# Optimization experiments

Measured on AMD Instinct MI355X. Metric: run time of the kernel, lower is better.

Reference implementation:

```python
import jax, jax.numpy as jnp
import numpy as np

B, T, S = 4, 2048, 2048
D, H, DFF = 1024, 16, 4096
HD = D // H
EPS = 1e-5


def layer_norm(x, gamma, beta):
    mean = x.mean(-1, keepdims=True)
    var = ((x - mean) ** 2).mean(-1, keepdims=True)
    return gamma * (x - mean) / jnp.sqrt(var + EPS) + beta


def attn(q, k, v):
    # q: [B,H,Tq,hd], k,v: [B,H,Tk,hd]
    scores = jnp.einsum('bhqd,bhkd->bhqk', q, k) / (HD ** 0.5)
    p = jax.nn.softmax(scores, axis=-1)
    return jnp.einsum('bhqk,bhkd->bhqd', p, v)


def split_heads(x, n_chunks):
    # x: [B,T,n_chunks*D] -> n_chunks tensors [B,H,T,hd] (matches torch reshape/chunk order)
    b, t, _ = x.shape
    x = x.reshape(b, t, H, n_chunks * HD).transpose(0, 2, 1, 3)
    return jnp.split(x, n_chunks, axis=-1)


def merge_heads(x):
    b, h, t, hd = x.shape
    return x.transpose(0, 2, 1, 3).reshape(b, t, h * hd)


def setup_inputs() -> dict:
    key = jax.random.key(0)
    ks = jax.random.split(key, 16)
    s = 0.02
    return {
        'x_enc': jax.random.normal(ks[0], (B, S, D), jnp.float32),
        'x_dec': jax.random.normal(ks[1], (B, T, D), jnp.float32),
        'qkv_w': jax.random.normal(ks[2], (D, 3 * D), jnp.float32) * s,
        'qkv_b': jnp.zeros((3 * D,), jnp.float32),
        'sa_o_w': jax.random.normal(ks[3], (D, D), jnp.float32) * s,
        'sa_o_b': jnp.zeros((D,), jnp.float32),
        'g1': jnp.ones((D,), jnp.float32),
        'be1': jnp.zeros((D,), jnp.float32),
        'q_w': jax.random.normal(ks[4], (D, D), jnp.float32) * s,
        'q_b': jnp.zeros((D,), jnp.float32),
        'kv_w': jax.random.normal(ks[5], (D, 2 * D), jnp.float32) * s,
        'kv_b': jnp.zeros((2 * D,), jnp.float32),
        'ca_o_w': jax.random.normal(ks[6], (D, D), jnp.float32) * s,
        'ca_o_b': jnp.zeros((D,), jnp.float32),
        'g2': jnp.ones((D,), jnp.float32),
        'be2': jnp.zeros((D,), jnp.float32),
        'ff_w1': jax.random.normal(ks[7], (D, DFF), jnp.float32) * s,
        'ff_b1': jnp.zeros((DFF,), jnp.float32),
        'ff_w2': jax.random.normal(ks[8], (DFF, D), jnp.float32) * s,
        'ff_b2': jnp.zeros((D,), jnp.float32),
        'g3': jnp.ones((D,), jnp.float32),
        'be3': jnp.zeros((D,), jnp.float32),
    }


def reference(x_enc, x_dec, qkv_w, qkv_b, sa_o_w, sa_o_b, g1, be1,
              q_w, q_b, kv_w, kv_b, ca_o_w, ca_o_b, g2, be2,
              ff_w1, ff_b1, ff_w2, ff_b2, g3, be3):
    # --- self attention on x_dec (dropout = identity at inference) ---
    qkv = x_dec @ qkv_w + qkv_b                      # [B,T,3D]
    q, k, v = split_heads(qkv, 3)
    sa = merge_heads(attn(q, k, v)) @ sa_o_w + sa_o_b
    res = layer_norm(sa + x_dec, g1, be1)
    # --- cross attention: q from decoder stream, kv from encoder ---
    kv = x_enc @ kv_w + kv_b                         # [B,S,2D]
    kc, vc = split_heads(kv, 2)
    qc, = split_heads(res @ q_w + q_b, 1)
    ca = merge_heads(attn(qc, kc, vc)) @ ca_o_w + ca_o_b
    res2 = layer_norm(ca + res, g2, be2)
    # --- feed forward ---
    ff = jax.nn.relu(res2 @ ff_w1 + ff_b1) @ ff_w2 + ff_b2
    return layer_norm(ff + res2, g3, be3)
```

## Files before the change

kernel.cpp:

```cpp
#include <hip/hip_runtime.h>

typedef unsigned short u16;
typedef unsigned int   u32;
typedef __bf16 bf16_t;
typedef bf16_t bf16x4 __attribute__((ext_vector_type(4)));
typedef bf16_t bf16x8 __attribute__((ext_vector_type(8)));
typedef float  f32x4  __attribute__((ext_vector_type(4)));

__device__ __forceinline__ u16 f2bf(float f) {
  u32 u = __builtin_bit_cast(u32, f);
  u32 r = u + 0x7fffu + ((u >> 16) & 1u);
  return (u16)(r >> 16);
}
__device__ __forceinline__ float bf2f(u16 h) {
  u32 u = ((u32)h) << 16;
  return __builtin_bit_cast(float, u);
}

__device__ __forceinline__ void gl_lds16(const u16* g, u16* l) {
  __builtin_amdgcn_global_load_lds(
      (const __attribute__((address_space(1))) u32*)g,
      (__attribute__((address_space(3))) u32*)l, 16, 0, 0);
}

__global__ __launch_bounds__(256) void k_cvt(const float* __restrict__ in,
                                             u16* __restrict__ out, long n4) {
  long i = (long)blockIdx.x * 256 + threadIdx.x;
  if (i >= n4) return;
  float4 v = reinterpret_cast<const float4*>(in)[i];
  ushort4 o;
  o.x = f2bf(v.x); o.y = f2bf(v.y); o.z = f2bf(v.z); o.w = f2bf(v.w);
  reinterpret_cast<ushort4*>(out)[i] = o;
}

__global__ __launch_bounds__(256) void k_transpose_cvt(const float* __restrict__ W,
                                                       u16* __restrict__ Wt,
                                                       int K, int N) {
  __shared__ u16 tile[32][33];
  int n0 = blockIdx.x * 32, k0 = blockIdx.y * 32;
  int tx = threadIdx.x & 31, ty = threadIdx.x >> 5;
#pragma unroll
  for (int i = 0; i < 4; ++i) {
    int k = ty + i * 8;
    tile[k][tx] = f2bf(W[(size_t)(k0 + k) * N + n0 + tx]);
  }
  __syncthreads();
#pragma unroll
  for (int i = 0; i < 4; ++i) {
    int n = ty + i * 8;
    Wt[(size_t)(n0 + n) * K + k0 + tx] = tile[tx][n];
  }
}

__global__ __launch_bounds__(256) void k_vtrans(const u16* __restrict__ in,
                                                u16* __restrict__ out,
                                                long long ibs, int ihs, int irs,
                                                int Tk) {
  __shared__ u16 t[64][72];
  const int tid = threadIdx.x;
  const int head = blockIdx.y;
  const int b = head >> 4, h = head & 15;
  const int kt = blockIdx.x * 64;
  const u16* ip = in + (size_t)b * ibs + (size_t)h * ihs;
  u16* op = out + (size_t)head * 64 * Tk;
#pragma unroll
  for (int i = 0; i < 2; ++i) {
    int c = i * 256 + tid;
    int key = c >> 3, d = (c & 7) * 8;
    *reinterpret_cast<uint4*>(&t[key][d]) =
        *reinterpret_cast<const uint4*>(ip + (size_t)(kt + key) * irs + d);
  }
  __syncthreads();
#pragma unroll
  for (int i = 0; i < 2; ++i) {
    int c = i * 256 + tid;
    int d = c >> 3, k8 = (c & 7) * 8;
    ushort4 lo, hi;
    lo.x = t[k8 + 0][d]; lo.y = t[k8 + 1][d]; lo.z = t[k8 + 2][d]; lo.w = t[k8 + 3][d];
    hi.x = t[k8 + 4][d]; hi.y = t[k8 + 5][d]; hi.z = t[k8 + 6][d]; hi.w = t[k8 + 7][d];
    uint4 o;
    o.x = ((u32)lo.y << 16) | lo.x; o.y = ((u32)lo.w << 16) | lo.z;
    o.z = ((u32)hi.y << 16) | hi.x; o.w = ((u32)hi.w << 16) | hi.z;
    *reinterpret_cast<uint4*>(op + (size_t)d * Tk + kt + k8) = o;
  }
}

template<int RELU>
__global__ __launch_bounds__(256) void k_gemm_bt(
    const u16* __restrict__ A, const u16* __restrict__ Bt,
    const float* __restrict__ bias, u16* __restrict__ C,
    int M, int N, int K)
{
  __shared__ __align__(16) u16 As[2][128 * 64];
  __shared__ __align__(16) u16 Bs[2][128 * 64];
  const int tid = threadIdx.x;
  const int lane = tid & 63, wid = tid >> 6;
  const int wr = wid >> 1, wc = wid & 1;
  const int l15 = lane & 15, g = lane >> 4;
  const int bm = blockIdx.x * 128, bn = blockIdx.y * 128;
  const int srow = lane >> 3, scol = (lane & 7) * 8;

  f32x4 acc[4][4] = {};

  auto stage = [&](int buf, int kt) {
#pragma unroll
    for (int i = 0; i < 4; ++i) {
      int ch = wid * 4 + i;
      gl_lds16(A  + (size_t)(bm + ch * 8 + srow) * K + kt + scol, &As[buf][ch * 512]);
      gl_lds16(Bt + (size_t)(bn + ch * 8 + srow) * K + kt + scol, &Bs[buf][ch * 512]);
    }
  };

  stage(0, 0);
  __syncthreads();
  int cur = 0;
  for (int kt = 0; kt < K; kt += 64) {
    if (kt + 64 < K) stage(cur ^ 1, kt + 64);
#pragma unroll
    for (int ks = 0; ks < 2; ++ks) {
      bf16x8 af[4], bfr[4];
#pragma unroll
      for (int m = 0; m < 4; ++m)
        af[m] = *reinterpret_cast<const bf16x8*>(&As[cur][(wr * 64 + m * 16 + l15) * 64 + ks * 32 + g * 8]);
#pragma unroll
      for (int n = 0; n < 4; ++n)
        bfr[n] = *reinterpret_cast<const bf16x8*>(&Bs[cur][(wc * 64 + n * 16 + l15) * 64 + ks * 32 + g * 8]);
      __builtin_amdgcn_s_setprio(1);
#pragma unroll
      for (int m = 0; m < 4; ++m)
#pragma unroll
        for (int n = 0; n < 4; ++n)
          acc[m][n] = __builtin_amdgcn_mfma_f32_16x16x32_bf16(af[m], bfr[n], acc[m][n], 0, 0, 0);
      __builtin_amdgcn_s_setprio(0);
    }
    __syncthreads();
    cur ^= 1;
  }
  float bv[4];
#pragma unroll
  for (int n = 0; n < 4; ++n) bv[n] = bias[bn + wc * 64 + n * 16 + l15];
#pragma unroll
  for (int m = 0; m < 4; ++m)
#pragma unroll
    for (int r = 0; r < 4; ++r) {
      int row = bm + wr * 64 + m * 16 + g * 4 + r;
#pragma unroll
      for (int n = 0; n < 4; ++n) {
        float v = acc[m][n][r] + bv[n];
        if (RELU) v = fmaxf(v, 0.f);
        C[(size_t)row * N + bn + wc * 64 + n * 16 + l15] = f2bf(v);
      }
    }
}

__global__ __launch_bounds__(256) void k_gemm_sk(
    const u16* __restrict__ A, const u16* __restrict__ Bt,
    float* __restrict__ P,
    int M, int N, int Kfull, int Kchunk)
{
  __shared__ __align__(16) u16 As[2][128 * 32];
  __shared__ __align__(16) u16 Bs[2][128 * 32];
  const int tid = threadIdx.x;
  const int lane = tid & 63, wid = tid >> 6;
  const int wr = wid >> 1, wc = wid & 1;
  const int l15 = lane & 15, g = lane >> 4;
  const int bm = blockIdx.x * 128, bn = blockIdx.y * 128;
  const int z = blockIdx.z;
  const int k0 = z * Kchunk;
  float* Pz = P + (size_t)z * M * N;
  const int srow = tid >> 2, scol = (tid & 3) * 8;

  f32x4 acc[4][4] = {};

  auto stage = [&](int buf, int kt) {
#pragma unroll
    for (int i = 0; i < 2; ++i) {
      int row = i * 64 + srow;
      gl_lds16(A  + (size_t)(bm + row) * Kfull + k0 + kt + scol, &As[buf][row * 32 + scol]);
      gl_lds16(Bt + (size_t)(bn + row) * Kfull + k0 + kt + scol, &Bs[buf][row * 32 + scol]);
    }
  };

  stage(0, 0);
  __syncthreads();
  int cur = 0;
  for (int kt = 0; kt < Kchunk; kt += 32) {
    if (kt + 32 < Kchunk) stage(cur ^ 1, kt + 32);
    bf16x8 af[4], bfr[4];
#pragma unroll
    for (int m = 0; m < 4; ++m)
      af[m] = *reinterpret_cast<const bf16x8*>(&As[cur][(wr * 64 + m * 16 + l15) * 32 + g * 8]);
#pragma unroll
    for (int n = 0; n < 4; ++n)
      bfr[n] = *reinterpret_cast<const bf16x8*>(&Bs[cur][(wc * 64 + n * 16 + l15) * 32 + g * 8]);
    __builtin_amdgcn_s_setprio(1);
#pragma unroll
    for (int m = 0; m < 4; ++m)
#pragma unroll
      for (int n = 0; n < 4; ++n)
        acc[m][n] = __builtin_amdgcn_mfma_f32_16x16x32_bf16(af[m], bfr[n], acc[m][n], 0, 0, 0);
    __builtin_amdgcn_s_setprio(0);
    __syncthreads();
    cur ^= 1;
  }
#pragma unroll
  for (int m = 0; m < 4; ++m)
#pragma unroll
    for (int r = 0; r < 4; ++r) {
      int row = bm + wr * 64 + m * 16 + g * 4 + r;
#pragma unroll
      for (int n = 0; n < 4; ++n)
        Pz[(size_t)row * N + bn + wc * 64 + n * 16 + l15] = acc[m][n][r];
    }
}

template<int RELU>
__global__ __launch_bounds__(512, 1) void k_gemm256(
    const u16* __restrict__ A, const u16* __restrict__ Bt,
    const float* __restrict__ bias, u16* __restrict__ C,
    int M, int N, int K)
{
  __shared__ __align__(16) u16 lds[65536];
  const int tid = threadIdx.x;
  const int lane = tid & 63, wid = tid >> 6;
  const int wr = wid >> 2, wc = wid & 3;
  const int l15 = lane & 15, g = lane >> 4;
  const int bm = blockIdx.x * 256, bn = blockIdx.y * 256;
  const int srow = tid >> 3;
  const int swcol = (((tid & 7) ^ ((tid >> 3) & 7)) * 8);
  const int swr = l15 & 7;

  f32x4 acc[8][4] = {};

  auto stageA = [&](int buf, int j, int kt) {
    gl_lds16(A + (size_t)(bm + j * 64 + srow) * K + kt + swcol,
             lds + buf * 32768 + j * 4096 + wid * 512);
  };
  auto stageB = [&](int buf, int j, int kt) {
    gl_lds16(Bt + (size_t)(bn + j * 64 + srow) * K + kt + swcol,
             lds + buf * 32768 + 16384 + j * 4096 + wid * 512);
  };

  stageB(0, 0, 0); stageB(0, 1, 0); stageB(0, 2, 0); stageB(0, 3, 0);
  stageA(0, 0, 0); stageA(0, 2, 0); stageA(0, 1, 0); stageA(0, 3, 0);
  asm volatile("s_waitcnt vmcnt(2)" ::: "memory");
  __builtin_amdgcn_s_barrier();

  int cur = 0;
  for (int kt = 0; kt < K; kt += 64) {
    const u16* Ab = lds + cur * 32768;
    const u16* Bb = lds + cur * 32768 + 16384;
    const bool pre = (kt + 64 < K);
    const int nb = cur ^ 1;
    bf16x8 af[4][2], bflo[2][2], bfhi[2][2];

#pragma unroll
    for (int m = 0; m < 4; ++m)
#pragma unroll
      for (int ks = 0; ks < 2; ++ks)
        af[m][ks] = *reinterpret_cast<const bf16x8*>(
            &Ab[(2 * wr) * 4096 + (m * 16 + l15) * 64 + (((ks * 4 + g) ^ swr) * 8)]);
#pragma unroll
    for (int n = 0; n < 2; ++n)
#pragma unroll
      for (int ks = 0; ks < 2; ++ks)
        bflo[n][ks] = *reinterpret_cast<const bf16x8*>(
            &Bb[wc * 4096 + (n * 16 + l15) * 64 + (((ks * 4 + g) ^ swr) * 8)]);
    if (pre) { stageB(nb, 0, kt + 64); stageB(nb, 1, kt + 64); }
    __builtin_amdgcn_s_setprio(1);
#pragma unroll
    for (int m = 0; m < 4; ++m)
#pragma unroll
      for (int n = 0; n < 2; ++n)
#pragma unroll
        for (int ks = 0; ks < 2; ++ks)
          acc[m][n] = __builtin_amdgcn_mfma_f32_16x16x32_bf16(af[m][ks], bflo[n][ks], acc[m][n], 0, 0, 0);
    __builtin_amdgcn_s_setprio(0);
    __builtin_amdgcn_s_barrier();

#pragma unroll
    for (int n = 0; n < 2; ++n)
#pragma unroll
      for (int ks = 0; ks < 2; ++ks)
        bfhi[n][ks] = *reinterpret_cast<const bf16x8*>(
            &Bb[wc * 4096 + ((n + 2) * 16 + l15) * 64 + (((ks * 4 + g) ^ swr) * 8)]);
    if (pre) { stageB(nb, 2, kt + 64); stageB(nb, 3, kt + 64); }
    __builtin_amdgcn_s_setprio(1);
#pragma unroll
    for (int m = 0; m < 4; ++m)
#pragma unroll
      for (int n = 0; n < 2; ++n)
#pragma unroll
        for (int ks = 0; ks < 2; ++ks)
          acc[m][n + 2] = __builtin_amdgcn_mfma_f32_16x16x32_bf16(af[m][ks], bfhi[n][ks], acc[m][n + 2], 0, 0, 0);
    __builtin_amdgcn_s_setprio(0);
    if (pre) { asm volatile("s_waitcnt vmcnt(4)" ::: "memory"); }
    else     { asm volatile("s_waitcnt vmcnt(0)" ::: "memory"); }
    __builtin_amdgcn_s_barrier();

#pragma unroll
    for (int m = 0; m < 4; ++m)
#pragma unroll
      for (int ks = 0; ks < 2; ++ks)
        af[m][ks] = *reinterpret_cast<const bf16x8*>(
            &Ab[(2 * wr + 1) * 4096 + (m * 16 + l15) * 64 + (((ks * 4 + g) ^ swr) * 8)]);
    if (pre) { stageA(nb, 0, kt + 64); stageA(nb, 2, kt + 64); }
    __builtin_amdgcn_s_setprio(1);
#pragma unroll
    for (int m = 0; m < 4; ++m)
#pragma unroll
      for (int n = 0; n < 2; ++n)
#pragma unroll
        for (int ks = 0; ks < 2; ++ks)
          acc[m + 4][n + 2] = __builtin_amdgcn_mfma_f32_16x16x32_bf16(af[m][ks], bfhi[n][ks], acc[m + 4][n + 2], 0, 0, 0);
    __builtin_amdgcn_s_setprio(0);
    __builtin_amdgcn_s_barrier();

    if (pre) { stageA(nb, 1, kt + 64); stageA(nb, 3, kt + 64); }
    __builtin_amdgcn_s_setprio(1);
#pragma unroll
    for (int m = 0; m < 4; ++m)
#pragma unroll
      for (int n = 0; n < 2; ++n)
#pragma unroll
        for (int ks = 0; ks < 2; ++ks)
          acc[m + 4][n] = __builtin_amdgcn_mfma_f32_16x16x32_bf16(af[m][ks], bflo[n][ks], acc[m + 4][n], 0, 0, 0);
    __builtin_amdgcn_s_setprio(0);
    asm volatile("s_waitcnt vmcnt(2)" ::: "memory");
    __builtin_amdgcn_s_barrier();
    cur ^= 1;
  }

  float bv[4];
#pragma unroll
  for (int n = 0; n < 4; ++n) bv[n] = bias[bn + wc * 64 + n * 16 + l15];
#pragma unroll
  for (int m = 0; m < 8; ++m)
#pragma unroll
    for (int r = 0; r < 4; ++r) {
      int row = bm + wr * 128 + m * 16 + g * 4 + r;
#pragma unroll
      for (int n = 0; n < 4; ++n) {
        float v = acc[m][n][r] + bv[n];
        if (RELU) v = fmaxf(v, 0.f);
        C[(size_t)row * N + bn + wc * 64 + n * 16 + l15] = f2bf(v);
      }
    }
}

__global__ __launch_bounds__(512) void k_flash2(
    const u16* __restrict__ Qg, const u16* __restrict__ Kg, const u16* __restrict__ VTg,
    u16* __restrict__ Og,
    long long qbs, int qhs, int qrs,
    long long kbs, int khs, int krs,
    long long obs, int ohs, int ors,
    int Tk)
{
  __shared__ __align__(16) u16 Ks[64][72];
  __shared__ __align__(16) u16 Vs[64][72];
  const int tid = threadIdx.x;
  const int lane = tid & 63, wid = tid >> 6;
  const int l15 = lane & 15, g = lane >> 4;
  const int head = blockIdx.x;
  const int b = head >> 4, h = head & 15;
  const int srow = tid >> 3, scol = (tid & 7) * 8;

  const u16* Q  = Qg + (size_t)b * qbs + (size_t)h * qhs;
  const u16* Kp = Kg + (size_t)b * kbs + (size_t)h * khs;
  const u16* Vp = VTg + (size_t)head * 64 * Tk;
  u16* Op = Og + (size_t)b * obs + (size_t)h * ohs;

  const int q0 = blockIdx.y * 256 + wid * 32;
  const float SCL = 0.125f * 1.44269504f;

  bf16x8 qf0[2], qf1[2];
#pragma unroll
  for (int ks = 0; ks < 2; ++ks) {
    bf16x8 r0 = *reinterpret_cast<const bf16x8*>(Q + (size_t)(q0 + l15) * qrs + ks * 32 + g * 8);
    bf16x8 r1 = *reinterpret_cast<const bf16x8*>(Q + (size_t)(q0 + 16 + l15) * qrs + ks * 32 + g * 8);
#pragma unroll
    for (int j = 0; j < 8; ++j) {
      qf0[ks][j] = (bf16_t)((float)r0[j] * SCL);
      qf1[ks][j] = (bf16_t)((float)r1[j] * SCL);
    }
  }
  bf16x8 ones;
#pragma unroll
  for (int j = 0; j < 8; ++j) ones[j] = (bf16_t)1.0f;

  f32x4 oacc0[4] = {}, oacc1[4] = {};
  f32x4 lacc0 = {}, lacc1 = {};

  uint4 ka, va, kb, vb;

  auto load_set = [&](int kt, uint4& k0, uint4& v0) {
    k0 = *reinterpret_cast<const uint4*>(Kp + (size_t)(kt + srow) * krs + scol);
    v0 = *reinterpret_cast<const uint4*>(Vp + (size_t)srow * Tk + kt + scol);
  };

  auto tile = [&](const uint4& k0, const uint4& v0,
                  int ktn, uint4& nk0, uint4& nv0) {
    __syncthreads();
    *reinterpret_cast<uint4*>(&Ks[srow][scol]) = k0;
    *reinterpret_cast<uint4*>(&Vs[srow][scol]) = v0;
    load_set(ktn, nk0, nv0);
    __syncthreads();

    f32x4 sc0[4] = {}, sc1[4] = {};
    __builtin_amdgcn_s_setprio(1);
#pragma unroll
    for (int ks = 0; ks < 2; ++ks)
#pragma unroll
      for (int kb2 = 0; kb2 < 4; ++kb2) {
        bf16x8 kf = *reinterpret_cast<const bf16x8*>(&Ks[kb2 * 16 + l15][ks * 32 + g * 8]);
        sc0[kb2] = __builtin_amdgcn_mfma_f32_16x16x32_bf16(kf, qf0[ks], sc0[kb2], 0, 0, 0);
        sc1[kb2] = __builtin_amdgcn_mfma_f32_16x16x32_bf16(kf, qf1[ks], sc1[kb2], 0, 0, 0);
      }
    __builtin_amdgcn_s_setprio(0);

    bf16x8 p0a, p0b, p1a, p1b;
#pragma unroll
    for (int r = 0; r < 4; ++r) {
      p0a[r]     = (bf16_t)__builtin_amdgcn_exp2f(sc0[0][r]);
      p0a[4 + r] = (bf16_t)__builtin_amdgcn_exp2f(sc0[1][r]);
      p0b[r]     = (bf16_t)__builtin_amdgcn_exp2f(sc0[2][r]);
      p0b[4 + r] = (bf16_t)__builtin_amdgcn_exp2f(sc0[3][r]);
      p1a[r]     = (bf16_t)__builtin_amdgcn_exp2f(sc1[0][r]);
      p1a[4 + r] = (bf16_t)__builtin_amdgcn_exp2f(sc1[1][r]);
      p1b[r]     = (bf16_t)__builtin_amdgcn_exp2f(sc1[2][r]);
      p1b[4 + r] = (bf16_t)__builtin_amdgcn_exp2f(sc1[3][r]);
    }

    __builtin_amdgcn_s_setprio(1);
#pragma unroll
    for (int kc = 0; kc < 2; ++kc) {
      const bf16x8& pf0 = kc ? p0b : p0a;
      const bf16x8& pf1 = kc ? p1b : p1a;
#pragma unroll
      for (int nb = 0; nb < 4; ++nb) {
        bf16x4 vlo = *reinterpret_cast<const bf16x4*>(&Vs[nb * 16 + l15][kc * 32 + 4 * g]);
        bf16x4 vhi = *reinterpret_cast<const bf16x4*>(&Vs[nb * 16 + l15][kc * 32 + 16 + 4 * g]);
        bf16x8 vf;
#pragma unroll
        for (int j = 0; j < 4; ++j) { vf[j] = vlo[j]; vf[4 + j] = vhi[j]; }
        oacc0[nb] = __builtin_amdgcn_mfma_f32_16x16x32_bf16(pf0, vf, oacc0[nb], 0, 0, 0);
        oacc1[nb] = __builtin_amdgcn_mfma_f32_16x16x32_bf16(pf1, vf, oacc1[nb], 0, 0, 0);
      }
      lacc0 = __builtin_amdgcn_mfma_f32_16x16x32_bf16(pf0, ones, lacc0, 0, 0, 0);
      lacc1 = __builtin_amdgcn_mfma_f32_16x16x32_bf16(pf1, ones, lacc1, 0, 0, 0);
    }
    __builtin_amdgcn_s_setprio(0);
  };

  load_set(0, ka, va);
  for (int kt = 0; kt < Tk; kt += 128) {
    tile(ka, va, kt + 64, kb, vb);
    int ktn = (kt + 128 < Tk) ? kt + 128 : 0;
    tile(kb, vb, ktn, ka, va);
  }

#pragma unroll
  for (int r = 0; r < 4; ++r) {
    float inv0 = 1.f / lacc0[r];
    float inv1 = 1.f / lacc1[r];
#pragma unroll
    for (int nb = 0; nb < 4; ++nb) {
      Op[(size_t)(q0 + g * 4 + r) * ors + nb * 16 + l15]      = f2bf(oacc0[nb][r] * inv0);
      Op[(size_t)(q0 + 16 + g * 4 + r) * ors + nb * 16 + l15] = f2bf(oacc1[nb][r] * inv1);
    }
  }
}

__device__ __forceinline__ void load4v(const float* p, float* v) {
  float4 t = *reinterpret_cast<const float4*>(p);
  v[0] = t.x; v[1] = t.y; v[2] = t.z; v[3] = t.w;
}
__device__ __forceinline__ void load4v(const u16* p, float* v) {
  ushort4 t = *reinterpret_cast<const ushort4*>(p);
  v[0] = bf2f(t.x); v[1] = bf2f(t.y); v[2] = bf2f(t.z); v[3] = bf2f(t.w);
}
__device__ __forceinline__ void store4v(float* p, const float* v) {
  float4 t; t.x = v[0]; t.y = v[1]; t.z = v[2]; t.w = v[3];
  *reinterpret_cast<float4*>(p) = t;
}
__device__ __forceinline__ void store4v(u16* p, const float* v) {
  ushort4 t; t.x = f2bf(v[0]); t.y = f2bf(v[1]); t.z = f2bf(v[2]); t.w = f2bf(v[3]);
  *reinterpret_cast<ushort4*>(p) = t;
}

__device__ __forceinline__ void ln_core(float* v, int tid, const float* gamma,
                                        const float* beta, float* o) {
  float s = v[0] + v[1] + v[2] + v[3];
  float q = v[0]*v[0] + v[1]*v[1] + v[2]*v[2] + v[3]*v[3];
#pragma unroll
  for (int off = 32; off > 0; off >>= 1) {
    s += __shfl_down(s, off);
    q += __shfl_down(q, off);
  }
  __shared__ float sh[8];
  const int lane = tid & 63, wid = tid >> 6;
  if (lane == 0) { sh[wid] = s; sh[4 + wid] = q; }
  __syncthreads();
  s = sh[0] + sh[1] + sh[2] + sh[3];
  q = sh[4] + sh[5] + sh[6] + sh[7];
  float mean = s * (1.f / 1024.f);
  float var = q * (1.f / 1024.f) - mean * mean;
  float inv = 1.f / sqrtf(var + 1e-5f);
  float gv[4], bv[4];
  load4v(gamma + tid * 4, gv);
  load4v(beta + tid * 4, bv);
#pragma unroll
  for (int j = 0; j < 4; ++j) o[j] = gv[j] * (v[j] - mean) * inv + bv[j];
}

template<typename TRES, typename TOUT>
__global__ __launch_bounds__(256) void k_add_ln(
    const u16* __restrict__ X, const TRES* __restrict__ R,
    const float* __restrict__ gamma, const float* __restrict__ beta,
    TOUT* __restrict__ Out)
{
  const int row = blockIdx.x;
  const int tid = threadIdx.x;
  const size_t base = (size_t)row * 1024 + tid * 4;
  float x[4], rr[4], v[4], o[4];
  load4v(X + base, x);
  load4v(R + base, rr);
#pragma unroll
  for (int j = 0; j < 4; ++j) v[j] = x[j] + rr[j];
  ln_core(v, tid, gamma, beta, o);
  store4v(Out + base, o);
}

__global__ __launch_bounds__(256) void k_add_ln_ff(
    const float* __restrict__ P0, const float* __restrict__ P1,
    const float* __restrict__ bias, const u16* __restrict__ R,
    const float* __restrict__ gamma, const float* __restrict__ beta,
    float* __restrict__ Out)
{
  const int row = blockIdx.x;
  const int tid = threadIdx.x;
  const size_t base = (size_t)row * 1024 + tid * 4;
  float p0[4], p1[4], bb[4], rr[4], v[4], o[4];
  load4v(P0 + base, p0);
  load4v(P1 + base, p1);
  load4v(bias + tid * 4, bb);
  load4v(R + base, rr);
#pragma unroll
  for (int j = 0; j < 4; ++j) v[j] = p0[j] + p1[j] + bb[j] + rr[j];
  ln_core(v, tid, gamma, beta, o);
  store4v(Out + base, o);
}

extern "C" void kernel_launch(void* const* d_in, const int* in_sizes, int n_in,
                              void* d_out, int out_size, void* d_ws, size_t ws_size,
                              hipStream_t stream)
{
  (void)in_sizes; (void)n_in; (void)out_size; (void)ws_size;
  const float* x_enc  = (const float*)d_in[0];
  const float* x_dec  = (const float*)d_in[1];
  const float* qkv_w  = (const float*)d_in[2];
  const float* qkv_b  = (const float*)d_in[3];
  const float* sa_o_w = (const float*)d_in[4];
  const float* sa_o_b = (const float*)d_in[5];
  const float* g1     = (const float*)d_in[6];
  const float* be1    = (const float*)d_in[7];
  const float* q_w    = (const float*)d_in[8];
  const float* q_b    = (const float*)d_in[9];
  const float* kv_w   = (const float*)d_in[10];
  const float* kv_b   = (const float*)d_in[11];
  const float* ca_o_w = (const float*)d_in[12];
  const float* ca_o_b = (const float*)d_in[13];
  const float* g2     = (const float*)d_in[14];
  const float* be2    = (const float*)d_in[15];
  const float* ff_w1  = (const float*)d_in[16];
  const float* ff_b1  = (const float*)d_in[17];
  const float* ff_w2  = (const float*)d_in[18];
  const float* ff_b2  = (const float*)d_in[19];
  const float* g3     = (const float*)d_in[20];
  const float* be3    = (const float*)d_in[21];
  float* out = (float*)d_out;

  u16* Wb = (u16*)d_ws;
  const size_t O_WQKV = 0;
  const size_t O_WSAO = O_WQKV + (size_t)3072 * 1024;
  const size_t O_WQ   = O_WSAO + (size_t)1024 * 1024;
  const size_t O_WKV  = O_WQ   + (size_t)1024 * 1024;
  const size_t O_WCAO = O_WKV  + (size_t)2048 * 1024;
  const size_t O_WFF1 = O_WCAO + (size_t)1024 * 1024;
  const size_t O_WFF2 = O_WFF1 + (size_t)4096 * 1024;
  const size_t O_XD   = O_WFF2 + (size_t)1024 * 4096;
  const size_t O_XE   = O_XD + 8388608;
  const size_t O_QKV  = O_XE + 8388608;
  const size_t O_QC   = O_QKV + 16777216;
  const size_t O_ATT  = O_QKV + 25165824;
  const size_t O_RES  = O_ATT + 8388608;
  const size_t O_RES2 = O_RES + 8388608;
  const size_t O_FF1  = O_RES2 + 8388608;
  const size_t O_VT   = O_FF1;
  const size_t O_VT2  = O_FF1 + 8388608;
  const size_t O_GO   = O_FF1 + 33554432;
  float* Pf = (float*)(Wb + O_QKV);

  k_cvt<<<8192, 256, 0, stream>>>(x_dec, Wb + O_XD, 2097152);
  k_cvt<<<8192, 256, 0, stream>>>(x_enc, Wb + O_XE, 2097152);
  k_transpose_cvt<<<dim3(96, 32),  256, 0, stream>>>(qkv_w,  Wb + O_WQKV, 1024, 3072);
  k_transpose_cvt<<<dim3(32, 32),  256, 0, stream>>>(sa_o_w, Wb + O_WSAO, 1024, 1024);
  k_transpose_cvt<<<dim3(32, 32),  256, 0, stream>>>(q_w,    Wb + O_WQ,   1024, 1024);
  k_transpose_cvt<<<dim3(64, 32),  256, 0, stream>>>(kv_w,   Wb + O_WKV,  1024, 2048);
  k_transpose_cvt<<<dim3(32, 32),  256, 0, stream>>>(ca_o_w, Wb + O_WCAO, 1024, 1024);
  k_transpose_cvt<<<dim3(128, 32), 256, 0, stream>>>(ff_w1,  Wb + O_WFF1, 1024, 4096);
  k_transpose_cvt<<<dim3(32, 128), 256, 0, stream>>>(ff_w2,  Wb + O_WFF2, 4096, 1024);

  k_gemm256<0><<<dim3(32, 12), 512, 0, stream>>>(Wb + O_XD, Wb + O_WQKV, qkv_b,
                                                 Wb + O_QKV, 8192, 3072, 1024);
  k_vtrans<<<dim3(32, 64), 256, 0, stream>>>(Wb + O_QKV + 128, Wb + O_VT,
                                             (long long)2048 * 3072, 192, 3072, 2048);
  k_flash2<<<dim3(64, 8), 512, 0, stream>>>(Wb + O_QKV, Wb + O_QKV + 64, Wb + O_VT,
                                            Wb + O_ATT,
                                            (long long)2048 * 3072, 192, 3072,
                                            (long long)2048 * 3072, 192, 3072,
                                            (long long)2048 * 1024, 64, 1024, 2048);
  k_gemm_bt<0><<<dim3(64, 8), 256, 0, stream>>>(Wb + O_ATT, Wb + O_WSAO, sa_o_b,
                                                Wb + O_GO, 8192, 1024, 1024);
  k_add_ln<float, u16><<<8192, 256, 0, stream>>>(Wb + O_GO, x_dec, g1, be1, Wb + O_RES);

  k_gemm256<0><<<dim3(32, 8), 512, 0, stream>>>(Wb + O_XE, Wb + O_WKV, kv_b,
                                                Wb + O_QKV, 8192, 2048, 1024);
  k_vtrans<<<dim3(32, 64), 256, 0, stream>>>(Wb + O_QKV + 64, Wb + O_VT2,
                                             (long long)2048 * 2048, 128, 2048, 2048);
  k_gemm_bt<0><<<dim3(64, 8), 256, 0, stream>>>(Wb + O_RES, Wb + O_WQ, q_b,
                                                Wb + O_QC, 8192, 1024, 1024);
  k_flash2<<<dim3(64, 8), 512, 0, stream>>>(Wb + O_QC, Wb + O_QKV, Wb + O_VT2,
                                            Wb + O_ATT,
                                            (long long)2048 * 1024, 64, 1024,
                                            (long long)2048 * 2048, 128, 2048,
                                            (long long)2048 * 1024, 64, 1024, 2048);
  k_gemm_bt<0><<<dim3(64, 8), 256, 0, stream>>>(Wb + O_ATT, Wb + O_WCAO, ca_o_b,
                                                Wb + O_GO, 8192, 1024, 1024);
  k_add_ln<u16, u16><<<8192, 256, 0, stream>>>(Wb + O_GO, Wb + O_RES, g2, be2, Wb + O_RES2);

  k_gemm256<1><<<dim3(32, 16), 512, 0, stream>>>(Wb + O_RES2, Wb + O_WFF1, ff_b1,
                                                 Wb + O_FF1, 8192, 4096, 1024);
  k_gemm_sk<<<dim3(64, 8, 2), 256, 0, stream>>>(Wb + O_FF1, Wb + O_WFF2, Pf,
                                                8192, 1024, 4096, 2048);
  k_add_ln_ff<<<8192, 256, 0, stream>>>(Pf, Pf + 8388608, ff_b2, Wb + O_RES2,
                                        g3, be3, out);
}
```

Baseline: 589.7 us.

## Replace FF2 split-K GEMM with 256x256-tile pipelined split-K kernel

Swaps the 128x128-tile split-K FF2 GEMM for a 256x256-tile variant that reuses the swizzled LDS layout and quarter-stage interleaved prefetch pipeline of the existing big GEMM. Larger tiles raise arithmetic intensity and cut global/LDS traffic per MFMA. The grid shrinks from 1024 to 256 blocks (one per CU with launch bounds 512,1), which risks poorer occupancy or tail balance.

```diff
diff --git a/kernel.cpp b/kernel.cpp
--- a/kernel.cpp
+++ b/kernel.cpp
@@ -150,67 +150,6 @@
         if (RELU) v = fmaxf(v, 0.f);
         C[(size_t)row * N + bn + wc * 64 + n * 16 + l15] = f2bf(v);
       }
-    }
-}
-
-__global__ __launch_bounds__(256) void k_gemm_sk(
-    const u16* __restrict__ A, const u16* __restrict__ Bt,
-    float* __restrict__ P,
-    int M, int N, int Kfull, int Kchunk)
-{
-  __shared__ __align__(16) u16 As[2][128 * 32];
-  __shared__ __align__(16) u16 Bs[2][128 * 32];
-  const int tid = threadIdx.x;
-  const int lane = tid & 63, wid = tid >> 6;
-  const int wr = wid >> 1, wc = wid & 1;
-  const int l15 = lane & 15, g = lane >> 4;
-  const int bm = blockIdx.x * 128, bn = blockIdx.y * 128;
-  const int z = blockIdx.z;
-  const int k0 = z * Kchunk;
-  float* Pz = P + (size_t)z * M * N;
-  const int srow = tid >> 2, scol = (tid & 3) * 8;
-
-  f32x4 acc[4][4] = {};
-
-  auto stage = [&](int buf, int kt) {
-#pragma unroll
-    for (int i = 0; i < 2; ++i) {
-      int row = i * 64 + srow;
-      gl_lds16(A  + (size_t)(bm + row) * Kfull + k0 + kt + scol, &As[buf][row * 32 + scol]);
-      gl_lds16(Bt + (size_t)(bn + row) * Kfull + k0 + kt + scol, &Bs[buf][row * 32 + scol]);
-    }
-  };
-
-  stage(0, 0);
-  __syncthreads();
-  int cur = 0;
-  for (int kt = 0; kt < Kchunk; kt += 32) {
-    if (kt + 32 < Kchunk) stage(cur ^ 1, kt + 32);
-    bf16x8 af[4], bfr[4];
-#pragma unroll
-    for (int m = 0; m < 4; ++m)
-      af[m] = *reinterpret_cast<const bf16x8*>(&As[cur][(wr * 64 + m * 16 + l15) * 32 + g * 8]);
-#pragma unroll
-    for (int n = 0; n < 4; ++n)
-      bfr[n] = *reinterpret_cast<const bf16x8*>(&Bs[cur][(wc * 64 + n * 16 + l15) * 32 + g * 8]);
-    __builtin_amdgcn_s_setprio(1);
-#pragma unroll
-    for (int m = 0; m < 4; ++m)
-#pragma unroll
-      for (int n = 0; n < 4; ++n)
-        acc[m][n] = __builtin_amdgcn_mfma_f32_16x16x32_bf16(af[m], bfr[n], acc[m][n], 0, 0, 0);
-    __builtin_amdgcn_s_setprio(0);
-    __syncthreads();
-    cur ^= 1;
-  }
-#pragma unroll
-  for (int m = 0; m < 4; ++m)
-#pragma unroll
-    for (int r = 0; r < 4; ++r) {
-      int row = bm + wr * 64 + m * 16 + g * 4 + r;
-#pragma unroll
-      for (int n = 0; n < 4; ++n)
-        Pz[(size_t)row * N + bn + wc * 64 + n * 16 + l15] = acc[m][n][r];
     }
 }
 
@@ -345,6 +284,135 @@
         if (RELU) v = fmaxf(v, 0.f);
         C[(size_t)row * N + bn + wc * 64 + n * 16 + l15] = f2bf(v);
       }
+    }
+}
+
+__global__ __launch_bounds__(512, 1) void k_gemm256sk(
+    const u16* __restrict__ A, const u16* __restrict__ Bt,
+    float* __restrict__ P,
+    int M, int N, int Kfull, int Kchunk)
+{
+  __shared__ __align__(16) u16 lds[65536];
+  const int tid = threadIdx.x;
+  const int lane = tid & 63, wid = tid >> 6;
+  const int wr = wid >> 2, wc = wid & 3;
+  const int l15 = lane & 15, g = lane >> 4;
+  const int bm = blockIdx.x * 256, bn = blockIdx.y * 256;
+  const int k0 = blockIdx.z * Kchunk;
+  float* Pz = P + (size_t)blockIdx.z * M * N;
+  const int srow = tid >> 3;
+  const int swcol = (((tid & 7) ^ ((tid >> 3) & 7)) * 8);
+  const int swr = l15 & 7;
+
+  f32x4 acc[8][4] = {};
+
+  auto stageA = [&](int buf, int j, int kt) {
+    gl_lds16(A + (size_t)(bm + j * 64 + srow) * Kfull + k0 + kt + swcol,
+             lds + buf * 32768 + j * 4096 + wid * 512);
+  };
+  auto stageB = [&](int buf, int j, int kt) {
+    gl_lds16(Bt + (size_t)(bn + j * 64 + srow) * Kfull + k0 + kt + swcol,
+             lds + buf * 32768 + 16384 + j * 4096 + wid * 512);
+  };
+
+  stageB(0, 0, 0); stageB(0, 1, 0); stageB(0, 2, 0); stageB(0, 3, 0);
+  stageA(0, 0, 0); stageA(0, 2, 0); stageA(0, 1, 0); stageA(0, 3, 0);
+  asm volatile("s_waitcnt vmcnt(2)" ::: "memory");
+  __builtin_amdgcn_s_barrier();
+
+  int cur = 0;
+  for (int kt = 0; kt < Kchunk; kt += 64) {
+    const u16* Ab = lds + cur * 32768;
+    const u16* Bb = lds + cur * 32768 + 16384;
+    const bool pre = (kt + 64 < Kchunk);
+    const int nb = cur ^ 1;
+    bf16x8 af[4][2], bflo[2][2], bfhi[2][2];
+
+#pragma unroll
+    for (int m = 0; m < 4; ++m)
+#pragma unroll
+      for (int ks = 0; ks < 2; ++ks)
+        af[m][ks] = *reinterpret_cast<const bf16x8*>(
+            &Ab[(2 * wr) * 4096 + (m * 16 + l15) * 64 + (((ks * 4 + g) ^ swr) * 8)]);
+#pragma unroll
+    for (int n = 0; n < 2; ++n)
+#pragma unroll
+      for (int ks = 0; ks < 2; ++ks)
+        bflo[n][ks] = *reinterpret_cast<const bf16x8*>(
+            &Bb[wc * 4096 + (n * 16 + l15) * 64 + (((ks * 4 + g) ^ swr) * 8)]);
+    if (pre) { stageB(nb, 0, kt + 64); stageB(nb, 1, kt + 64); }
+    __builtin_amdgcn_s_setprio(1);
+#pragma unroll
+    for (int m = 0; m < 4; ++m)
+#pragma unroll
+      for (int n = 0; n < 2; ++n)
+#pragma unroll
+        for (int ks = 0; ks < 2; ++ks)
+          acc[m][n] = __builtin_amdgcn_mfma_f32_16x16x32_bf16(af[m][ks], bflo[n][ks], acc[m][n], 0, 0, 0);
+    __builtin_amdgcn_s_setprio(0);
+    __builtin_amdgcn_s_barrier();
+
+#pragma unroll
+    for (int n = 0; n < 2; ++n)
+#pragma unroll
+      for (int ks = 0; ks < 2; ++ks)
+        bfhi[n][ks] = *reinterpret_cast<const bf16x8*>(
+            &Bb[wc * 4096 + ((n + 2) * 16 + l15) * 64 + (((ks * 4 + g) ^ swr) * 8)]);
+    if (pre) { stageB(nb, 2, kt + 64); stageB(nb, 3, kt + 64); }
+    __builtin_amdgcn_s_setprio(1);
+#pragma unroll
+    for (int m = 0; m < 4; ++m)
+#pragma unroll
+      for (int n = 0; n < 2; ++n)
+#pragma unroll
+        for (int ks = 0; ks < 2; ++ks)
+          acc[m][n + 2] = __builtin_amdgcn_mfma_f32_16x16x32_bf16(af[m][ks], bfhi[n][ks], acc[m][n + 2], 0, 0, 0);
+    __builtin_amdgcn_s_setprio(0);
+    if (pre) { asm volatile("s_waitcnt vmcnt(4)" ::: "memory"); }
+    else     { asm volatile("s_waitcnt vmcnt(0)" ::: "memory"); }
+    __builtin_amdgcn_s_barrier();
+
+#pragma unroll
+    for (int m = 0; m < 4; ++m)
+#pragma unroll
+      for (int ks = 0; ks < 2; ++ks)
+        af[m][ks] = *reinterpret_cast<const bf16x8*>(
+            &Ab[(2 * wr + 1) * 4096 + (m * 16 + l15) * 64 + (((ks * 4 + g) ^ swr) * 8)]);
+    if (pre) { stageA(nb, 0, kt + 64); stageA(nb, 2, kt + 64); }
+    __builtin_amdgcn_s_setprio(1);
+#pragma unroll
+    for (int m = 0; m < 4; ++m)
+#pragma unroll
+      for (int n = 0; n < 2; ++n)
+#pragma unroll
+        for (int ks = 0; ks < 2; ++ks)
+          acc[m + 4][n + 2] = __builtin_amdgcn_mfma_f32_16x16x32_bf16(af[m][ks], bfhi[n][ks], acc[m + 4][n + 2], 0, 0, 0);
+    __builtin_amdgcn_s_setprio(0);
+    __builtin_amdgcn_s_barrier();
+
+    if (pre) { stageA(nb, 1, kt + 64); stageA(nb, 3, kt + 64); }
+    __builtin_amdgcn_s_setprio(1);
+#pragma unroll
+    for (int m = 0; m < 4; ++m)
+#pragma unroll
+      for (int n = 0; n < 2; ++n)
+#pragma unroll
+        for (int ks = 0; ks < 2; ++ks)
+          acc[m + 4][n] = __builtin_amdgcn_mfma_f32_16x16x32_bf16(af[m][ks], bflo[n][ks], acc[m + 4][n], 0, 0, 0);
+    __builtin_amdgcn_s_setprio(0);
+    asm volatile("s_waitcnt vmcnt(2)" ::: "memory");
+    __builtin_amdgcn_s_barrier();
+    cur ^= 1;
+  }
+
+#pragma unroll
+  for (int m = 0; m < 8; ++m)
+#pragma unroll
+    for (int r = 0; r < 4; ++r) {
+      int row = bm + wr * 128 + m * 16 + g * 4 + r;
+#pragma unroll
+      for (int n = 0; n < 4; ++n)
+        Pz[(size_t)row * N + bn + wc * 64 + n * 16 + l15] = acc[m][n][r];
     }
 }
 
@@ -641,8 +709,8 @@
 
   k_gemm256<1><<<dim3(32, 16), 512, 0, stream>>>(Wb + O_RES2, Wb + O_WFF1, ff_b1,
                                                  Wb + O_FF1, 8192, 4096, 1024);
-  k_gemm_sk<<<dim3(64, 8, 2), 256, 0, stream>>>(Wb + O_FF1, Wb + O_WFF2, Pf,
-                                                8192, 1024, 4096, 2048);
+  k_gemm256sk<<<dim3(32, 4, 2), 512, 0, stream>>>(Wb + O_FF1, Wb + O_WFF2, Pf,
+                                                  8192, 1024, 4096, 2048);
   k_add_ln_ff<<<8192, 256, 0, stream>>>(Pf, Pf + 8388608, ff_b2, Wb + O_RES2,
                                         g3, be3, out);
 }
```

After: 568.8 us (median of 2 runs). -3.5%, faster.
